# Kernel optimization log

Hardware: AMD Instinct MI355X
Metric: run time of the kernel (lower is better)

The kernel has to match this reference:

```python
import jax, jax.numpy as jnp
import numpy as np

B, T, I, H = 16, 2048, 512, 512

def setup_inputs() -> dict:
    key = jax.random.key(0)
    k_x, k_wi, k_wr, k_uz = jax.random.split(key, 4)
    inputs = jax.random.normal(k_x, (B, T, I), dtype=jnp.float32)
    W_in = jax.random.normal(k_wi, (H, I), dtype=jnp.float32) / (I ** 0.5)
    b_in = jnp.zeros((H,), dtype=jnp.float32)
    W_rec = jax.random.normal(k_wr, (H, H), dtype=jnp.float32) / (H ** 0.5)
    U_z = jax.random.normal(k_uz, (H, H), dtype=jnp.float32) / (H ** 0.5)
    b_u = jnp.zeros((H,), dtype=jnp.float32)
    return {"inputs": inputs, "W_in": W_in, "b_in": b_in, "W_rec": W_rec, "U_z": U_z, "b_u": b_u}

def reference(inputs, W_in, b_in, W_rec, U_z, b_u):
    # Precompute the input-dependent candidate z for all timesteps in one GEMM:
    # z_t = tanh(x_t @ W_in^T + b_in) has no recurrent dependency.
    z_all = jnp.tanh(jnp.einsum('bti,hi->bth', inputs, W_in) + b_in)  # (B,T,H)
    # Recurrent gated blend must be sequential -> lax.scan over time.
    def step(state, z_t):
        u = jax.nn.sigmoid(state @ W_rec.T + z_t @ U_z.T + b_u)  # (B,H)
        new_state = u * state + (1.0 - u) * z_t
        return new_state, new_state
    init = jnp.zeros((inputs.shape[0], W_rec.shape[0]), dtype=inputs.dtype)
    _, outs = jax.lax.scan(step, init, jnp.swapaxes(z_all, 0, 1))  # scan over T
    return jnp.swapaxes(outs, 0, 1)  # (B,T,H)
```

## Files before the change

kernel.cpp:

```cpp
#include <hip/hip_runtime.h>
#include <cmath>

#define BB 16
#define TT 2048
#define II 512
#define HH 512
#define NSL 4
#define RS  128
#define SCAN_THREADS 512

template<int ACT>
__global__ __launch_bounds__(256) void gemm_nt(const float* __restrict__ A,
                                               const float* __restrict__ B,
                                               const float* __restrict__ bias,
                                               float* __restrict__ C,
                                               int M, int N, int K)
{
    __shared__ float As[16][132];
    __shared__ float Bs[16][132];

    const int m0  = blockIdx.x * 128;
    const int n0  = blockIdx.y * 128;
    const int tid = threadIdx.x;
    const int tm  = tid & 15;
    const int tn  = tid >> 4;

    float acc[8][8];
#pragma unroll
    for (int i = 0; i < 8; ++i)
#pragma unroll
        for (int jj = 0; jj < 8; ++jj) acc[i][jj] = 0.f;

    const int lr = tid >> 1;
    const int lh = (tid & 1) * 8;

    for (int k0 = 0; k0 < K; k0 += 16) {
        const float4* ap = (const float4*)&A[(size_t)(m0 + lr) * K + k0 + lh];
        float4 a0 = ap[0], a1 = ap[1];
        const float4* bp = (const float4*)&B[(size_t)(n0 + lr) * K + k0 + lh];
        float4 b0 = bp[0], b1 = bp[1];

        __syncthreads();
        As[lh + 0][lr] = a0.x; As[lh + 1][lr] = a0.y; As[lh + 2][lr] = a0.z; As[lh + 3][lr] = a0.w;
        As[lh + 4][lr] = a1.x; As[lh + 5][lr] = a1.y; As[lh + 6][lr] = a1.z; As[lh + 7][lr] = a1.w;
        Bs[lh + 0][lr] = b0.x; Bs[lh + 1][lr] = b0.y; Bs[lh + 2][lr] = b0.z; Bs[lh + 3][lr] = b0.w;
        Bs[lh + 4][lr] = b1.x; Bs[lh + 5][lr] = b1.y; Bs[lh + 6][lr] = b1.z; Bs[lh + 7][lr] = b1.w;
        __syncthreads();

#pragma unroll
        for (int kk = 0; kk < 16; ++kk) {
            float4 av0 = *(const float4*)&As[kk][tm * 8];
            float4 av1 = *(const float4*)&As[kk][tm * 8 + 4];
            float4 bv0 = *(const float4*)&Bs[kk][tn * 8];
            float4 bv1 = *(const float4*)&Bs[kk][tn * 8 + 4];
            const float ar[8] = {av0.x, av0.y, av0.z, av0.w, av1.x, av1.y, av1.z, av1.w};
            const float br[8] = {bv0.x, bv0.y, bv0.z, bv0.w, bv1.x, bv1.y, bv1.z, bv1.w};
#pragma unroll
            for (int i = 0; i < 8; ++i)
#pragma unroll
                for (int jj = 0; jj < 8; ++jj)
                    acc[i][jj] = fmaf(ar[i], br[jj], acc[i][jj]);
        }
    }

    float bias_r[8];
#pragma unroll
    for (int jj = 0; jj < 8; ++jj) bias_r[jj] = bias[n0 + tn * 8 + jj];

#pragma unroll
    for (int i = 0; i < 8; ++i) {
        const int m = m0 + tm * 8 + i;
        float o[8];
#pragma unroll
        for (int jj = 0; jj < 8; ++jj) {
            float v = acc[i][jj] + bias_r[jj];
            o[jj] = (ACT == 1) ? tanhf(v) : v;
        }
        float4* cp = (float4*)&C[(size_t)m * N + n0 + tn * 8];
        cp[0] = make_float4(o[0], o[1], o[2], o[3]);
        cp[1] = make_float4(o[4], o[5], o[6], o[7]);
    }
}

__global__ __launch_bounds__(SCAN_THREADS, 2) void scan_kernel(
    const float* __restrict__ W_rec,
    const float* __restrict__ a_all,
    float* __restrict__ zout,
    unsigned long long* __restrict__ htag)
{
    __shared__ float hs[HH];
    __shared__ float zs[RS];
    __shared__ float as_[RS];
    __shared__ float part[NSL][RS];
    __shared__ float hown[RS];

    const int tid = threadIdx.x;
    const int b   = blockIdx.x >> 2;
    const int s   = blockIdx.x & 3;
    const int j0  = s * RS;
    const int j   = tid & (RS - 1);
    const int p   = tid >> 7;
    const bool own = (tid >= j0) && (tid < j0 + RS);

    float w[128];
    {
        const float4* src = (const float4*)&W_rec[(size_t)(j0 + j) * HH + p * 128];
#pragma unroll
        for (int i = 0; i < 32; ++i) {
            float4 v = src[i];
            w[4 * i + 0] = v.x; w[4 * i + 1] = v.y;
            w[4 * i + 2] = v.z; w[4 * i + 3] = v.w;
        }
    }
    if (tid < RS) hown[tid] = 0.f;
    __syncthreads();

    const size_t hbase = (size_t)b * HH;

    for (int t = 0; t < TT; ++t) {
        const size_t rowoff = ((size_t)b * TT + t) * HH + j0;
        float zv = 0.f, av = 0.f;
        if (tid < RS) {
            zv = zout[rowoff + tid];
            av = a_all[rowoff + tid];
        }

        if (own) {
            hs[tid] = hown[tid - j0];
        } else {
            const unsigned long long* hp =
                &htag[(size_t)(t & 1) * BB * HH + hbase + tid];
            const unsigned int want = (unsigned int)t;
            unsigned long long v = __hip_atomic_load(hp, __ATOMIC_RELAXED,
                                                     __HIP_MEMORY_SCOPE_AGENT);
            while ((unsigned int)(v >> 32) != want) {
                __builtin_amdgcn_s_sleep(1);
                v = __hip_atomic_load(hp, __ATOMIC_RELAXED,
                                      __HIP_MEMORY_SCOPE_AGENT);
            }
            hs[tid] = __uint_as_float((unsigned int)v);
        }
        if (tid < RS) { zs[tid] = zv; as_[tid] = av; }
        __syncthreads();

        float acc = 0.f;
        {
            const float4* hv4 = (const float4*)&hs[p * 128];
#pragma unroll
            for (int i = 0; i < 32; ++i) {
                float4 hv = hv4[i];
                acc = fmaf(w[4 * i + 0], hv.x, acc);
                acc = fmaf(w[4 * i + 1], hv.y, acc);
                acc = fmaf(w[4 * i + 2], hv.z, acc);
                acc = fmaf(w[4 * i + 3], hv.w, acc);
            }
        }
        part[p][j] = acc;
        __syncthreads();

        if (tid < RS) {
            float v  = part[0][tid] + part[1][tid] + part[2][tid] + part[3][tid]
                     + as_[tid];
            float u  = 1.f / (1.f + expf(-v));
            float hp = hs[j0 + tid];
            float z  = zs[tid];
            float hn = fmaf(u, hp - z, z);
            hown[tid] = hn;
            unsigned long long pack =
                ((unsigned long long)(unsigned int)(t + 1) << 32) |
                (unsigned long long)__float_as_uint(hn);
            __hip_atomic_store(&htag[(size_t)((t + 1) & 1) * BB * HH + hbase + j0 + tid],
                               pack, __ATOMIC_RELAXED, __HIP_MEMORY_SCOPE_AGENT);
            zout[rowoff + tid] = hn;
        }
        __syncthreads();
    }
}

extern "C" void kernel_launch(void* const* d_in, const int* in_sizes, int n_in,
                              void* d_out, int out_size, void* d_ws, size_t ws_size,
                              hipStream_t stream)
{
    const float* X     = (const float*)d_in[0];
    const float* W_in  = (const float*)d_in[1];
    const float* b_in  = (const float*)d_in[2];
    const float* W_rec = (const float*)d_in[3];
    const float* U_z   = (const float*)d_in[4];
    const float* b_u   = (const float*)d_in[5];
    float* out = (float*)d_out;

    float* a_all = (float*)d_ws;
    unsigned long long* htag =
        (unsigned long long*)((char*)d_ws + (size_t)BB * TT * HH * 4);

    hipMemsetAsync(htag, 0, (size_t)2 * BB * HH * 8, stream);

    dim3 blk(256);
    dim3 g1(BB * TT / 128, HH / 128);
    gemm_nt<1><<<g1, blk, 0, stream>>>(X, W_in, b_in, out, BB * TT, HH, II);
    gemm_nt<0><<<g1, blk, 0, stream>>>(out, U_z, b_u, a_all, BB * TT, HH, HH);
    scan_kernel<<<dim3(BB * NSL), dim3(SCAN_THREADS), 0, stream>>>(W_rec, a_all, out, htag);
}
```

Measured before the change: 4.005 ms.

## Co-locate batch slices on one XCD and poll with sc0 loads when colocated

```diff
diff --git a/kernel.cpp b/kernel.cpp
--- a/kernel.cpp
+++ b/kernel.cpp
@@ -82,26 +82,56 @@
     }
 }
 
+__device__ __forceinline__ unsigned long long load_b64_sc0(const unsigned long long* p)
+{
+    unsigned long long v;
+    asm volatile("global_load_dwordx2 %0, %1, off sc0\n\t"
+                 "s_waitcnt vmcnt(0)"
+                 : "=v"(v) : "v"(p) : "memory");
+    return v;
+}
+
 __global__ __launch_bounds__(SCAN_THREADS, 2) void scan_kernel(
     const float* __restrict__ W_rec,
     const float* __restrict__ a_all,
     float* __restrict__ zout,
-    unsigned long long* __restrict__ htag)
+    unsigned long long* __restrict__ htag,
+    unsigned int* __restrict__ xtab)
 {
     __shared__ float hs[HH];
     __shared__ float zs[RS];
     __shared__ float as_[RS];
     __shared__ float part[NSL][RS];
     __shared__ float hown[RS];
+    __shared__ int   fs_sh;
 
     const int tid = threadIdx.x;
-    const int b   = blockIdx.x >> 2;
-    const int s   = blockIdx.x & 3;
+    const int bid = blockIdx.x;
+    const int b   = bid & 15;
+    const int s   = bid >> 4;
     const int j0  = s * RS;
     const int j   = tid & (RS - 1);
     const int p   = tid >> 7;
     const bool own = (tid >= j0) && (tid < j0 + RS);
 
+    unsigned int myxcc = 0;
+    asm volatile("s_getreg_b32 %0, hwreg(20, 0, 32)" : "=s"(myxcc));
+    if (tid == 0)
+        __hip_atomic_store(&xtab[bid], 0x80000000u | (myxcc & 0xFFFFu),
+                           __ATOMIC_RELAXED, __HIP_MEMORY_SCOPE_AGENT);
+    if (tid == 0) {
+        unsigned int ids[NSL];
+        for (int q = 0; q < NSL; ++q) {
+            unsigned int e;
+            do {
+                e = __hip_atomic_load(&xtab[q * BB + b], __ATOMIC_RELAXED,
+                                      __HIP_MEMORY_SCOPE_AGENT);
+            } while (!(e & 0x80000000u));
+            ids[q] = e;
+        }
+        fs_sh = (ids[0] == ids[1] && ids[1] == ids[2] && ids[2] == ids[3]) ? 1 : 0;
+    }
+
     float w[128];
     {
         const float4* src = (const float4*)&W_rec[(size_t)(j0 + j) * HH + p * 128];
@@ -114,6 +144,7 @@
     }
     if (tid < RS) hown[tid] = 0.f;
     __syncthreads();
+    const bool fastpath = (fs_sh != 0);
 
     const size_t hbase = (size_t)b * HH;
 
@@ -131,12 +162,14 @@
             const unsigned long long* hp =
                 &htag[(size_t)(t & 1) * BB * HH + hbase + tid];
             const unsigned int want = (unsigned int)t;
-            unsigned long long v = __hip_atomic_load(hp, __ATOMIC_RELAXED,
-                                                     __HIP_MEMORY_SCOPE_AGENT);
-            while ((unsigned int)(v >> 32) != want) {
-                __builtin_amdgcn_s_sleep(1);
-                v = __hip_atomic_load(hp, __ATOMIC_RELAXED,
-                                      __HIP_MEMORY_SCOPE_AGENT);
+            unsigned long long v;
+            int k = 0;
+            for (;;) {
+                if (fastpath && k < 4) v = load_b64_sc0(hp);
+                else                   v = __hip_atomic_load(hp, __ATOMIC_RELAXED,
+                                                             __HIP_MEMORY_SCOPE_AGENT);
+                if ((unsigned int)(v >> 32) == want) break;
+                if (++k > 2) __builtin_amdgcn_s_sleep(1);
             }
             hs[tid] = __uint_as_float((unsigned int)v);
         }
@@ -192,12 +225,14 @@
     float* a_all = (float*)d_ws;
     unsigned long long* htag =
         (unsigned long long*)((char*)d_ws + (size_t)BB * TT * HH * 4);
-
-    hipMemsetAsync(htag, 0, (size_t)2 * BB * HH * 8, stream);
+    unsigned int* xtab =
+        (unsigned int*)((char*)htag + (size_t)2 * BB * HH * 8);
+
+    hipMemsetAsync(htag, 0, (size_t)2 * BB * HH * 8 + 64 * 4, stream);
 
     dim3 blk(256);
     dim3 g1(BB * TT / 128, HH / 128);
     gemm_nt<1><<<g1, blk, 0, stream>>>(X, W_in, b_in, out, BB * TT, HH, II);
     gemm_nt<0><<<g1, blk, 0, stream>>>(out, U_z, b_u, a_all, BB * TT, HH, HH);
-    scan_kernel<<<dim3(BB * NSL), dim3(SCAN_THREADS), 0, stream>>>(W_rec, a_all, out, htag);
-}
+    scan_kernel<<<dim3(BB * NSL), dim3(SCAN_THREADS), 0, stream>>>(W_rec, a_all, out, htag, xtab);
+}
```

Measured after the change: 4.540 ms. 1.13x slower.
